# Performance work log

Hardware: AMD Instinct MI355X
Metric: run time of the kernel (lower is better)

The kernel has to match this reference:

```python
import jax, jax.numpy as jnp
import numpy as np

B, D, DFF, E, TOPK = 16384, 512, 2048, 8, 2


def setup_inputs() -> dict:
    key = jax.random.key(0)
    ks = jax.random.split(key, 5)
    scale_g = 1.0 / np.sqrt(D)
    scale_1 = 1.0 / np.sqrt(D)
    scale_2 = 1.0 / np.sqrt(DFF)
    return {
        "x": jax.random.normal(ks[0], (B, D), dtype=jnp.float32),
        "Wg": jax.random.normal(ks[1], (D, E), dtype=jnp.float32) * scale_g,
        "W1": jax.random.normal(ks[2], (E, D, DFF), dtype=jnp.float32) * scale_1,
        "b1": jnp.zeros((E, DFF), dtype=jnp.float32),
        "W2": jax.random.normal(ks[3], (E, DFF, D), dtype=jnp.float32) * scale_2,
        "b2": jnp.zeros((E, D), dtype=jnp.float32),
    }


def reference(x, Wg, W1, b1, W2, b2):
    # --- gate: top-k softmax routing weights, zeros elsewhere ---
    logits = x @ Wg                              # [B, E]
    probs = jax.nn.softmax(logits, axis=-1)      # [B, E]
    vals, idx = jax.lax.top_k(probs, TOPK)       # [B, K], [B, K]
    routing = jnp.zeros_like(probs).at[jnp.arange(x.shape[0])[:, None], idx].set(vals)  # [B, E]

    # --- experts: dense FFN per expert (equivalent math to masked dispatch) ---
    # original: gather selected tokens per expert, compute, scatter into
    # zeros[E, B, D], multiply by routing.T[:, :, None], sum over experts.
    # routing weight is exactly 0 for unselected tokens, so the dense form
    # out = sum_e routing[b, e] * expert_e(x_b) computes identical results.
    h = jax.nn.relu(jnp.einsum('bd,edf->ebf', x, W1) + b1[:, None, :])  # [E, B, DFF]
    y = jnp.einsum('ebf,efd->ebd', h, W2) + b2[:, None, :]              # [E, B, D]
    out = jnp.einsum('ebd,be->bd', y, routing)                          # [B, D]
    return out
```

## Files before the change

### kernel.cpp

```cpp
#include <hip/hip_runtime.h>
#include <stdint.h>

#define BTOK 16384
#define DM   512
#define DFF  2048
#define NE   8
#define NPAIR (BTOK*2)
#define BM 128
#define MAXTE 48

typedef short s16x8 __attribute__((ext_vector_type(8)));
typedef float f32x4 __attribute__((ext_vector_type(4)));

__device__ __forceinline__ uint16_t f2b(float f) {
  uint32_t u = __float_as_uint(f);
  u += 0x7fff + ((u >> 16) & 1);
  return (uint16_t)(u >> 16);
}

__device__ __forceinline__ void g2l16(const void* gp, void* lp) {
  __builtin_amdgcn_global_load_lds(
      (__attribute__((address_space(1))) void*)(void*)gp,
      (__attribute__((address_space(3))) void*)lp, 16, 0, 0);
}

__global__ void k_tr(const float* __restrict__ w1, const float* __restrict__ w2,
                     uint16_t* __restrict__ w1t, uint16_t* __restrict__ w2t) {
  __shared__ float t[32][33];
  int z = blockIdx.z, bx = blockIdx.x;
  int R, C, c0, r0;
  const float* src;
  uint16_t* dst;
  if (z < 8) { R = DM; C = DFF; c0 = (bx & 63) * 32; r0 = (bx >> 6) * 32;
               src = w1 + (size_t)z * R * C; dst = w1t + (size_t)z * R * C; }
  else       { R = DFF; C = DM; c0 = (bx & 15) * 32; r0 = (bx >> 4) * 32;
               src = w2 + (size_t)(z - 8) * R * C; dst = w2t + (size_t)(z - 8) * R * C; }
  int tx = threadIdx.x, ty = threadIdx.y;
#pragma unroll
  for (int j = 0; j < 4; j++)
    t[ty + j * 8][tx] = src[(size_t)(r0 + ty + j * 8) * C + c0 + tx];
  __syncthreads();
#pragma unroll
  for (int j = 0; j < 4; j++)
    dst[(size_t)(c0 + ty + j * 8) * R + r0 + tx] = f2b(t[tx][ty + j * 8]);
}

__global__ __launch_bounds__(256) void k_route(const float* __restrict__ x,
                                               const float* __restrict__ wg,
                                               int* __restrict__ counts,
                                               int* __restrict__ tk_e, float* __restrict__ tk_w,
                                               uint16_t* __restrict__ xb) {
  __shared__ int hist[NE];
  int tid = threadIdx.x, lane = tid & 63, wave = tid >> 6;
  if (tid < NE) hist[tid] = 0;
  __syncthreads();

  float wv[8][8];
#pragma unroll
  for (int j = 0; j < 8; j++) {
    const float4* wr = (const float4*)(wg + (size_t)(j * 64 + lane) * NE);
    float4 a = wr[0], b = wr[1];
    wv[j][0] = a.x; wv[j][1] = a.y; wv[j][2] = a.z; wv[j][3] = a.w;
    wv[j][4] = b.x; wv[j][5] = b.y; wv[j][6] = b.z; wv[j][7] = b.w;
  }

  int tok0 = blockIdx.x * 64 + wave * 16;
  for (int tt = 0; tt < 16; tt++) {
    int tok = tok0 + tt;
    const float* xr = x + (size_t)tok * DM;
    float xv[8];
#pragma unroll
    for (int j = 0; j < 8; j++) xv[j] = xr[j * 64 + lane];
    float acc[NE];
#pragma unroll
    for (int e = 0; e < NE; e++) acc[e] = 0.f;
#pragma unroll
    for (int j = 0; j < 8; j++)
#pragma unroll
      for (int e = 0; e < NE; e++) acc[e] += xv[j] * wv[j][e];
#pragma unroll
    for (int e = 0; e < NE; e++) {
#pragma unroll
      for (int off = 32; off > 0; off >>= 1) acc[e] += __shfl_xor(acc[e], off, 64);
    }
    if (lane == 0) {
      float mx = acc[0];
      for (int e = 1; e < NE; e++) mx = fmaxf(mx, acc[e]);
      float p[NE], s = 0.f;
      for (int e = 0; e < NE; e++) { p[e] = __expf(acc[e] - mx); s += p[e]; }
      float inv = 1.f / s;
      int e0 = 0; float v0 = p[0];
      for (int e = 1; e < NE; e++) if (p[e] > v0) { v0 = p[e]; e0 = e; }
      int e1 = -1; float v1 = -1.f;
      for (int e = 0; e < NE; e++) if (e != e0 && p[e] > v1) { v1 = p[e]; e1 = e; }
      tk_e[tok * 2]     = e0; tk_w[tok * 2]     = v0 * inv;
      tk_e[tok * 2 + 1] = e1; tk_w[tok * 2 + 1] = v1 * inv;
      atomicAdd(&hist[e0], 1);
      atomicAdd(&hist[e1], 1);
    }
  }
  const float* xs = x + (size_t)blockIdx.x * 32768;
  uint16_t* xd = xb + (size_t)blockIdx.x * 32768;
#pragma unroll
  for (int i = 0; i < 16; i++) {
    int o = i * 2048 + tid * 8;
    float4 a = *(const float4*)(xs + o);
    float4 b = *(const float4*)(xs + o + 4);
    uint16_t v[8] = {f2b(a.x), f2b(a.y), f2b(a.z), f2b(a.w),
                     f2b(b.x), f2b(b.y), f2b(b.z), f2b(b.w)};
    *(s16x8*)(xd + o) = *(s16x8*)v;
  }
  __syncthreads();
  if (tid < NE) atomicAdd(&counts[tid], hist[tid]);
}

__global__ void k_setup(const int* __restrict__ counts, int* __restrict__ offsets,
                        int* __restrict__ tile_r0, int* __restrict__ tcnt, int* __restrict__ tstart) {
  if (threadIdx.x != 0 || blockIdx.x != 0) return;
  int off = 0;
  for (int e = 0; e < NE; e++) { offsets[e] = off; off += counts[e]; }
  offsets[NE] = off;
  int nt = 0;
  for (int e = 0; e < NE; e++) {
    tstart[e] = nt;
    int c = 0;
    for (int r = offsets[e]; r < offsets[e + 1]; r += BM) { tile_r0[nt] = r; nt++; c++; }
    tcnt[e] = c;
  }
}

__global__ __launch_bounds__(256) void k_build(const int* __restrict__ tk_e, const float* __restrict__ tk_w,
                                               const int* __restrict__ offsets, int* __restrict__ cursors,
                                               int* __restrict__ tok_of, float* __restrict__ w_of,
                                               int* __restrict__ inv) {
  __shared__ int lcnt[NE], lbase[NE];
  int tid = threadIdx.x;
  int i = blockIdx.x * 256 + tid;
  if (tid < NE) lcnt[tid] = 0;
  __syncthreads();
  int e = tk_e[i];
  int local = atomicAdd(&lcnt[e], 1);
  __syncthreads();
  if (tid < NE) lbase[tid] = atomicAdd(&cursors[tid], lcnt[tid]);
  __syncthreads();
  int slot = offsets[e] + lbase[e] + local;
  tok_of[slot] = i >> 1;
  w_of[slot] = tk_w[i];
  inv[i] = slot;
}


__global__ __launch_bounds__(256, 2) void k_gemm1(
    const uint16_t* __restrict__ xb, const uint16_t* __restrict__ w1t,
    const float* __restrict__ b1,
    const int* __restrict__ tok_of, const int* __restrict__ offsets,
    const int* __restrict__ tile_r0, const int* __restrict__ tcnt, const int* __restrict__ tstart,
    uint16_t* __restrict__ h) {
  __shared__ uint16_t smem[24576];
  int id = blockIdx.x;
  int e = id & 7, j = id >> 3;
  int ti = j >> 3;
  if (ti >= tcnt[e]) return;
  int row0 = tile_r0[tstart[e] + ti], end = offsets[e + 1];
  int n0 = (j & 7) * 256;
  int tid = threadIdx.x, lane = tid & 63, wave = tid >> 6;
  int wr = (wave >> 1) * 64, wcb = (wave & 1) * 128;

  int aof[2];
#pragma unroll
  for (int it = 0; it < 2; it++) {
    int ci = it * 256 + tid;
    int row = ci >> 2;
    int c = (ci & 3) ^ ((row >> 1) & 3);
    int slot = row0 + row; if (slot >= end) slot = end - 1;
    aof[it] = tok_of[slot] * DM + c * 8;
  }
  int bof[4];
#pragma unroll
  for (int it = 0; it < 4; it++) {
    int ci = it * 256 + tid;
    int row = ci >> 2;
    int c = (ci & 3) ^ ((row >> 1) & 3);
    bof[it] = row * DM + c * 8;
  }
  const uint16_t* bb = w1t + (size_t)e * DFF * DM + (size_t)n0 * DM;
  int sfrag = (lane >> 4) ^ ((lane >> 1) & 3);

  f32x4 acc[4][8];
#pragma unroll
  for (int r = 0; r < 4; r++)
#pragma unroll
    for (int c = 0; c < 8; c++)
#pragma unroll
      for (int i = 0; i < 4; i++) acc[r][c][i] = 0.f;

#pragma unroll
  for (int it = 0; it < 2; it++)
    g2l16(xb + aof[it], smem + (size_t)(it * 256 + wave * 64) * 8);
#pragma unroll
  for (int it = 0; it < 4; it++)
    g2l16(bb + bof[it], smem + 4096 + (size_t)(it * 256 + wave * 64) * 8);

  int p = 0;
  for (int k0 = 0; k0 < DM; k0 += 32) {
    __syncthreads();
    int kn = k0 + 32, q = p ^ 1;
    if (kn < DM) {
#pragma unroll
      for (int it = 0; it < 2; it++)
        g2l16(xb + aof[it] + kn, smem + (size_t)q * 12288 + (size_t)(it * 256 + wave * 64) * 8);
#pragma unroll
      for (int it = 0; it < 4; it++)
        g2l16(bb + bof[it] + kn, smem + (size_t)q * 12288 + 4096 + (size_t)(it * 256 + wave * 64) * 8);
    }
    const uint16_t* sA = smem + (size_t)p * 12288;
    const uint16_t* sB = sA + 4096;
    s16x8 af[4], bf[8];
#pragma unroll
    for (int r = 0; r < 4; r++)
      af[r] = *(const s16x8*)(sA + (wr + r * 16 + (lane & 15)) * 32 + sfrag * 8);
#pragma unroll
    for (int c = 0; c < 8; c++)
      bf[c] = *(const s16x8*)(sB + (wcb + c * 16 + (lane & 15)) * 32 + sfrag * 8);
#pragma unroll
    for (int r = 0; r < 4; r++)
#pragma unroll
      for (int c = 0; c < 8; c++)
        acc[r][c] = __builtin_amdgcn_mfma_f32_16x16x32_bf16(af[r], bf[c], acc[r][c], 0, 0, 0);
    p = q;
  }
  __syncthreads();

  float bv[8];
#pragma unroll
  for (int c = 0; c < 8; c++) bv[c] = b1[(size_t)e * DFF + n0 + wcb + c * 16 + (lane & 15)];
#pragma unroll
  for (int ch = 0; ch < 2; ch++) {
    uint16_t* myreg = smem + wave * 4096;
#pragma unroll
    for (int r = 0; r < 4; r++)
#pragma unroll
      for (int c2 = 0; c2 < 4; c2++) {
        int gc = ch * 4 + c2;
#pragma unroll
        for (int i = 0; i < 4; i++) {
          int row = r * 16 + (lane >> 4) * 4 + i;
          int col = c2 * 16 + (lane & 15);
          float v = fmaxf(acc[r][gc][i] + bv[gc], 0.f);
          myreg[row * 64 + col] = f2b(v);
        }
      }
    __syncthreads();
#pragma unroll
    for (int it = 0; it < 8; it++) {
      int chunk = it * 256 + tid;
      int row = chunk >> 4, rem = chunk & 15;
      int strip = rem >> 3, cw = (rem & 7) * 8;
      int slot = row0 + row;
      if (slot < end) {
        const uint16_t* src = smem + ((row >> 6) * 2 + strip) * 4096 + (row & 63) * 64 + cw;
        *(s16x8*)(h + (size_t)slot * DFF + n0 + strip * 128 + ch * 64 + cw) = *(const s16x8*)src;
      }
    }
    __syncthreads();
  }
}

__global__ __launch_bounds__(256, 2) void k_gemm2(
    const uint16_t* __restrict__ h, const uint16_t* __restrict__ w2t,
    const float* __restrict__ b2,
    const float* __restrict__ w_of,
    const int* __restrict__ offsets,
    const int* __restrict__ tile_r0, const int* __restrict__ tcnt, const int* __restrict__ tstart,
    float* __restrict__ y32) {
  __shared__ uint16_t smem[24576];
  int id = blockIdx.x;
  int e = id & 7, j = id >> 3;
  int ti = j >> 1;
  if (ti >= tcnt[e]) return;
  int row0 = tile_r0[tstart[e] + ti], end = offsets[e + 1];
  int n0 = (j & 1) * 256;
  int tid = threadIdx.x, lane = tid & 63, wave = tid >> 6;
  int wr = (wave >> 1) * 64, wcb = (wave & 1) * 128;

  int aof[2];
#pragma unroll
  for (int it = 0; it < 2; it++) {
    int ci = it * 256 + tid;
    int row = ci >> 2;
    int c = (ci & 3) ^ ((row >> 1) & 3);
    int slot = row0 + row; if (slot >= end) slot = end - 1;
    aof[it] = slot * DFF + c * 8;
  }
  int bof[4];
#pragma unroll
  for (int it = 0; it < 4; it++) {
    int ci = it * 256 + tid;
    int row = ci >> 2;
    int c = (ci & 3) ^ ((row >> 1) & 3);
    bof[it] = row * DFF + c * 8;
  }
  const uint16_t* bb = w2t + (size_t)e * DM * DFF + (size_t)n0 * DFF;
  int sfrag = (lane >> 4) ^ ((lane >> 1) & 3);

  f32x4 acc[4][8];
#pragma unroll
  for (int r = 0; r < 4; r++)
#pragma unroll
    for (int c = 0; c < 8; c++)
#pragma unroll
      for (int i = 0; i < 4; i++) acc[r][c][i] = 0.f;

#pragma unroll
  for (int it = 0; it < 2; it++)
    g2l16(h + aof[it], smem + (size_t)(it * 256 + wave * 64) * 8);
#pragma unroll
  for (int it = 0; it < 4; it++)
    g2l16(bb + bof[it], smem + 4096 + (size_t)(it * 256 + wave * 64) * 8);

  int p = 0;
  for (int k0 = 0; k0 < DFF; k0 += 32) {
    __syncthreads();
    int kn = k0 + 32, q = p ^ 1;
    if (kn < DFF) {
#pragma unroll
      for (int it = 0; it < 2; it++)
        g2l16(h + aof[it] + kn, smem + (size_t)q * 12288 + (size_t)(it * 256 + wave * 64) * 8);
#pragma unroll
      for (int it = 0; it < 4; it++)
        g2l16(bb + bof[it] + kn, smem + (size_t)q * 12288 + 4096 + (size_t)(it * 256 + wave * 64) * 8);
    }
    const uint16_t* sA = smem + (size_t)p * 12288;
    const uint16_t* sB = sA + 4096;
    s16x8 af[4], bf[8];
#pragma unroll
    for (int r = 0; r < 4; r++)
      af[r] = *(const s16x8*)(sA + (wr + r * 16 + (lane & 15)) * 32 + sfrag * 8);
#pragma unroll
    for (int c = 0; c < 8; c++)
      bf[c] = *(const s16x8*)(sB + (wcb + c * 16 + (lane & 15)) * 32 + sfrag * 8);
#pragma unroll
    for (int r = 0; r < 4; r++)
#pragma unroll
      for (int c = 0; c < 8; c++)
        acc[r][c] = __builtin_amdgcn_mfma_f32_16x16x32_bf16(af[r], bf[c], acc[r][c], 0, 0, 0);
    p = q;
  }

  float bv[8];
#pragma unroll
  for (int c = 0; c < 8; c++) bv[c] = b2[(size_t)e * DM + n0 + wcb + c * 16 + (lane & 15)];
#pragma unroll
  for (int r = 0; r < 4; r++)
#pragma unroll
    for (int i = 0; i < 4; i++) {
      int rowg = wr + r * 16 + (lane >> 4) * 4 + i;
      int slot = row0 + rowg;
      if (slot < end) {
        float wgt = w_of[slot];
        size_t base = (size_t)slot * DM + n0 + wcb + (lane & 15);
#pragma unroll
        for (int c = 0; c < 8; c++) y32[base + c * 16] = wgt * (acc[r][c][i] + bv[c]);
      }
    }
}

__global__ __launch_bounds__(256) void k_combine(const float* __restrict__ y32,
                                                 const int* __restrict__ inv,
                                                 float* __restrict__ out) {
  int tid = threadIdx.x;
  int tok = blockIdx.x * 2 + (tid >> 7);
  int c4 = (tid & 127) * 4;
  int s0 = inv[tok * 2], s1 = inv[tok * 2 + 1];
  const float4 a = *(const float4*)(y32 + (size_t)s0 * DM + c4);
  const float4 b = *(const float4*)(y32 + (size_t)s1 * DM + c4);
  *(float4*)(out + (size_t)tok * DM + c4) = make_float4(a.x + b.x, a.y + b.y, a.z + b.z, a.w + b.w);
}

extern "C" void kernel_launch(void* const* d_in, const int* in_sizes, int n_in,
                              void* d_out, int out_size, void* d_ws, size_t ws_size,
                              hipStream_t stream) {
  const float* x  = (const float*)d_in[0];
  const float* wg = (const float*)d_in[1];
  const float* w1 = (const float*)d_in[2];
  const float* b1 = (const float*)d_in[3];
  const float* w2 = (const float*)d_in[4];
  const float* b2 = (const float*)d_in[5];
  float* out = (float*)d_out;

  char* ws = (char*)d_ws;
  const size_t MB = 1024 * 1024;
  uint16_t* xb   = (uint16_t*)ws;
  uint16_t* w1t  = (uint16_t*)(ws + 16 * MB);
  uint16_t* w2t  = (uint16_t*)(ws + 32 * MB);
  uint16_t* hbuf = (uint16_t*)(ws + 48 * MB);
  int* ctrl = (int*)(ws + 176 * MB);
  int*   counts  = ctrl;
  int*   cursors = ctrl + 8;
  int*   offsets = ctrl + 16;
  int*   tcnt    = ctrl + 32;
  int*   tstart  = ctrl + 40;
  int*   tile_r0 = ctrl + 48;
  int*   tk_e    = ctrl + 512;
  float* tk_w    = (float*)(ctrl + 512 + 32768);
  int*   tok_of  = ctrl + 512 + 2 * 32768;
  float* w_of    = (float*)(ctrl + 512 + 3 * 32768);
  int*   inv     = ctrl + 512 + 4 * 32768;
  float* y32     = (float*)(ws + 177 * MB);

  hipMemsetAsync(counts, 0, 16 * sizeof(int), stream);

  k_route<<<BTOK / 64, 256, 0, stream>>>(x, wg, counts, tk_e, tk_w, xb);
  k_tr<<<dim3(1024, 1, 16), dim3(32, 8), 0, stream>>>(w1, w2, w1t, w2t);
  k_setup<<<1, 64, 0, stream>>>(counts, offsets, tile_r0, tcnt, tstart);
  k_build<<<NPAIR / 256, 256, 0, stream>>>(tk_e, tk_w, offsets, cursors, tok_of, w_of, inv);
  k_gemm1<<<NE * MAXTE * 8, 256, 0, stream>>>(xb, w1t, b1, tok_of, offsets,
                                              tile_r0, tcnt, tstart, hbuf);
  k_gemm2<<<NE * MAXTE * 2, 256, 0, stream>>>(hbuf, w2t, b2, w_of, offsets,
                                              tile_r0, tcnt, tstart, y32);
  k_combine<<<BTOK / 2, 256, 0, stream>>>(y32, inv, out);
}
```

Measured before the change: 390.7 us.

## Rewrite expert GEMMs with 512-thread blocks, 4-stage LDS pipeline, larger tiles

Both grouped GEMMs move to 512-thread blocks with 8 waves. The global-to-LDS prefetch grows to a 4-stage ring with explicit vmcnt/lgkmcnt waits, split MFMA phases and raised priority around the MFMAs. GEMM1 now uses 256-row token tiles (a separate tile table is built in setup), while GEMM2 keeps 128 rows but spreads them over more waves. The aim is to hide memory latency and improve operand reuse in exchange for more LDS, hand-tuned wait counts, and more padding waste on partial expert tiles.

```diff
diff --git a/kernel.cpp b/kernel.cpp
--- a/kernel.cpp
+++ b/kernel.cpp
@@ -6,8 +6,8 @@
 #define DFF  2048
 #define NE   8
 #define NPAIR (BTOK*2)
-#define BM 128
-#define MAXTE 48
+#define MAXTA 24
+#define MAXTB 48
 
 typedef short s16x8 __attribute__((ext_vector_type(8)));
 typedef float f32x4 __attribute__((ext_vector_type(4)));
@@ -115,17 +115,23 @@
 }
 
 __global__ void k_setup(const int* __restrict__ counts, int* __restrict__ offsets,
-                        int* __restrict__ tile_r0, int* __restrict__ tcnt, int* __restrict__ tstart) {
+                        int* __restrict__ trA, int* __restrict__ tcntA, int* __restrict__ tstartA,
+                        int* __restrict__ trB, int* __restrict__ tcntB, int* __restrict__ tstartB) {
   if (threadIdx.x != 0 || blockIdx.x != 0) return;
   int off = 0;
   for (int e = 0; e < NE; e++) { offsets[e] = off; off += counts[e]; }
   offsets[NE] = off;
   int nt = 0;
   for (int e = 0; e < NE; e++) {
-    tstart[e] = nt;
-    int c = 0;
-    for (int r = offsets[e]; r < offsets[e + 1]; r += BM) { tile_r0[nt] = r; nt++; c++; }
-    tcnt[e] = c;
+    tstartA[e] = nt; int c = 0;
+    for (int r = offsets[e]; r < offsets[e + 1]; r += 256) { trA[nt++] = r; c++; }
+    tcntA[e] = c;
+  }
+  int nb = 0;
+  for (int e = 0; e < NE; e++) {
+    tstartB[e] = nb; int c = 0;
+    for (int r = offsets[e]; r < offsets[e + 1]; r += 128) { trB[nb++] = r; c++; }
+    tcntB[e] = c;
   }
 }
 
@@ -150,219 +156,273 @@
 }
 
 
-__global__ __launch_bounds__(256, 2) void k_gemm1(
+#define LDS16(off) (*(const s16x8*)((const char*)smem + (off)))
+#define VM8 asm volatile("s_waitcnt vmcnt(8)" ::: "memory")
+#define VM6 asm volatile("s_waitcnt vmcnt(6)" ::: "memory")
+#define VM4 asm volatile("s_waitcnt vmcnt(4)" ::: "memory")
+#define VM3 asm volatile("s_waitcnt vmcnt(3)" ::: "memory")
+#define VM0 asm volatile("s_waitcnt vmcnt(0)" ::: "memory")
+#define NOVM do{}while(0)
+#define NOSTG do{}while(0)
+#define MFMA16 __builtin_amdgcn_mfma_f32_16x16x32_bf16
+
+#define DS0_1(bb) do{ \
+  bf0 = LDS16(offB0 + (bb)*32768); bf1 = LDS16(offB1 + (bb)*32768); \
+  bf2 = LDS16(offB2 + (bb)*32768); bf3 = LDS16(offB3 + (bb)*32768); \
+  af0 = LDS16(offA0 + (bb)*32768); af1 = LDS16(offA1 + (bb)*32768); \
+  af2 = LDS16(offA2 + (bb)*32768); af3 = LDS16(offA3 + (bb)*32768); }while(0)
+#define DS1_1(bb) do{ \
+  af0 = LDS16(offA0 + (bb)*32768 + 4096); af1 = LDS16(offA1 + (bb)*32768 + 4096); \
+  af2 = LDS16(offA2 + (bb)*32768 + 4096); af3 = LDS16(offA3 + (bb)*32768 + 4096); }while(0)
+#define SA_1(bb) do{ \
+  g2l16(gA0, (char*)smem + (bb)*32768 + wave*1024); \
+  g2l16(gA1, (char*)smem + (bb)*32768 + 8192 + wave*1024); \
+  gA0 += 32; gA1 += 32; }while(0)
+#define SB_1(bb) do{ \
+  g2l16(gB0, (char*)smem + (bb)*32768 + 16384 + wave*1024); \
+  g2l16(gB1, (char*)smem + (bb)*32768 + 24576 + wave*1024); \
+  gB0 += 32; gB1 += 32; }while(0)
+#define MM16(H) do{ \
+  __builtin_amdgcn_s_setprio(1); \
+  acc[4*(H)+0][0] = MFMA16(af0, bf0, acc[4*(H)+0][0], 0, 0, 0); \
+  acc[4*(H)+1][0] = MFMA16(af1, bf0, acc[4*(H)+1][0], 0, 0, 0); \
+  acc[4*(H)+2][0] = MFMA16(af2, bf0, acc[4*(H)+2][0], 0, 0, 0); \
+  acc[4*(H)+3][0] = MFMA16(af3, bf0, acc[4*(H)+3][0], 0, 0, 0); \
+  acc[4*(H)+0][1] = MFMA16(af0, bf1, acc[4*(H)+0][1], 0, 0, 0); \
+  acc[4*(H)+1][1] = MFMA16(af1, bf1, acc[4*(H)+1][1], 0, 0, 0); \
+  acc[4*(H)+2][1] = MFMA16(af2, bf1, acc[4*(H)+2][1], 0, 0, 0); \
+  acc[4*(H)+3][1] = MFMA16(af3, bf1, acc[4*(H)+3][1], 0, 0, 0); \
+  acc[4*(H)+0][2] = MFMA16(af0, bf2, acc[4*(H)+0][2], 0, 0, 0); \
+  acc[4*(H)+1][2] = MFMA16(af1, bf2, acc[4*(H)+1][2], 0, 0, 0); \
+  acc[4*(H)+2][2] = MFMA16(af2, bf2, acc[4*(H)+2][2], 0, 0, 0); \
+  acc[4*(H)+3][2] = MFMA16(af3, bf2, acc[4*(H)+3][2], 0, 0, 0); \
+  acc[4*(H)+0][3] = MFMA16(af0, bf3, acc[4*(H)+0][3], 0, 0, 0); \
+  acc[4*(H)+1][3] = MFMA16(af1, bf3, acc[4*(H)+1][3], 0, 0, 0); \
+  acc[4*(H)+2][3] = MFMA16(af2, bf3, acc[4*(H)+2][3], 0, 0, 0); \
+  acc[4*(H)+3][3] = MFMA16(af3, bf3, acc[4*(H)+3][3], 0, 0, 0); \
+  __builtin_amdgcn_s_setprio(0); }while(0)
+#define TILE1(bb, SA, SB, VMX) do{ \
+  DS0_1(bb); SA; \
+  __builtin_amdgcn_s_barrier(); \
+  asm volatile("s_waitcnt lgkmcnt(0)" ::: "memory"); \
+  MM16(0); \
+  __builtin_amdgcn_s_barrier(); \
+  DS1_1(bb); SB; \
+  __builtin_amdgcn_s_barrier(); \
+  asm volatile("s_waitcnt lgkmcnt(0)" ::: "memory"); \
+  MM16(1); \
+  VMX; \
+  __builtin_amdgcn_s_barrier(); }while(0)
+
+__global__ __launch_bounds__(512, 2) void k_gemm1(
     const uint16_t* __restrict__ xb, const uint16_t* __restrict__ w1t,
     const float* __restrict__ b1,
     const int* __restrict__ tok_of, const int* __restrict__ offsets,
-    const int* __restrict__ tile_r0, const int* __restrict__ tcnt, const int* __restrict__ tstart,
+    const int* __restrict__ trA, const int* __restrict__ tcntA, const int* __restrict__ tstartA,
     uint16_t* __restrict__ h) {
-  __shared__ uint16_t smem[24576];
+  __shared__ __align__(16) uint16_t smem[65536];
   int id = blockIdx.x;
   int e = id & 7, j = id >> 3;
   int ti = j >> 3;
-  if (ti >= tcnt[e]) return;
-  int row0 = tile_r0[tstart[e] + ti], end = offsets[e + 1];
+  if (ti >= tcntA[e]) return;
+  int row0 = trA[tstartA[e] + ti], end = offsets[e + 1];
   int n0 = (j & 7) * 256;
   int tid = threadIdx.x, lane = tid & 63, wave = tid >> 6;
-  int wr = (wave >> 1) * 64, wcb = (wave & 1) * 128;
-
-  int aof[2];
-#pragma unroll
-  for (int it = 0; it < 2; it++) {
-    int ci = it * 256 + tid;
-    int row = ci >> 2;
-    int c = (ci & 3) ^ ((row >> 1) & 3);
-    int slot = row0 + row; if (slot >= end) slot = end - 1;
-    aof[it] = tok_of[slot] * DM + c * 8;
-  }
-  int bof[4];
-#pragma unroll
-  for (int it = 0; it < 4; it++) {
-    int ci = it * 256 + tid;
-    int row = ci >> 2;
-    int c = (ci & 3) ^ ((row >> 1) & 3);
-    bof[it] = row * DM + c * 8;
-  }
-  const uint16_t* bb = w1t + (size_t)e * DFF * DM + (size_t)n0 * DM;
-  int sfrag = (lane >> 4) ^ ((lane >> 1) & 3);
-
-  f32x4 acc[4][8];
-#pragma unroll
-  for (int r = 0; r < 4; r++)
-#pragma unroll
-    for (int c = 0; c < 8; c++)
-#pragma unroll
-      for (int i = 0; i < 4; i++) acc[r][c][i] = 0.f;
-
-#pragma unroll
-  for (int it = 0; it < 2; it++)
-    g2l16(xb + aof[it], smem + (size_t)(it * 256 + wave * 64) * 8);
-#pragma unroll
-  for (int it = 0; it < 4; it++)
-    g2l16(bb + bof[it], smem + 4096 + (size_t)(it * 256 + wave * 64) * 8);
-
-  int p = 0;
-  for (int k0 = 0; k0 < DM; k0 += 32) {
-    __syncthreads();
-    int kn = k0 + 32, q = p ^ 1;
-    if (kn < DM) {
-#pragma unroll
-      for (int it = 0; it < 2; it++)
-        g2l16(xb + aof[it] + kn, smem + (size_t)q * 12288 + (size_t)(it * 256 + wave * 64) * 8);
-#pragma unroll
-      for (int it = 0; it < 4; it++)
-        g2l16(bb + bof[it] + kn, smem + (size_t)q * 12288 + 4096 + (size_t)(it * 256 + wave * 64) * 8);
-    }
-    const uint16_t* sA = smem + (size_t)p * 12288;
-    const uint16_t* sB = sA + 4096;
-    s16x8 af[4], bf[8];
-#pragma unroll
-    for (int r = 0; r < 4; r++)
-      af[r] = *(const s16x8*)(sA + (wr + r * 16 + (lane & 15)) * 32 + sfrag * 8);
-#pragma unroll
-    for (int c = 0; c < 8; c++)
-      bf[c] = *(const s16x8*)(sB + (wcb + c * 16 + (lane & 15)) * 32 + sfrag * 8);
-#pragma unroll
-    for (int r = 0; r < 4; r++)
-#pragma unroll
-      for (int c = 0; c < 8; c++)
-        acc[r][c] = __builtin_amdgcn_mfma_f32_16x16x32_bf16(af[r], bf[c], acc[r][c], 0, 0, 0);
-    p = q;
-  }
-  __syncthreads();
-
-  float bv[8];
-#pragma unroll
-  for (int c = 0; c < 8; c++) bv[c] = b1[(size_t)e * DFF + n0 + wcb + c * 16 + (lane & 15)];
-#pragma unroll
-  for (int ch = 0; ch < 2; ch++) {
-    uint16_t* myreg = smem + wave * 4096;
-#pragma unroll
-    for (int r = 0; r < 4; r++)
-#pragma unroll
-      for (int c2 = 0; c2 < 4; c2++) {
-        int gc = ch * 4 + c2;
+  int wm = wave >> 2, wn = wave & 3;
+  int l15 = lane & 15, l4 = lane >> 4;
+
+  int offA0, offA1, offA2, offA3, offB0, offB1, offB2, offB3;
+  { int r;
+    r = wm*128 + 0*16 + l15; offA0 = r*64 + ((l4 ^ ((r>>1)&3)) << 4);
+    r = wm*128 + 1*16 + l15; offA1 = r*64 + ((l4 ^ ((r>>1)&3)) << 4);
+    r = wm*128 + 2*16 + l15; offA2 = r*64 + ((l4 ^ ((r>>1)&3)) << 4);
+    r = wm*128 + 3*16 + l15; offA3 = r*64 + ((l4 ^ ((r>>1)&3)) << 4);
+    r = wn*64  + 0*16 + l15; offB0 = 16384 + r*64 + ((l4 ^ ((r>>1)&3)) << 4);
+    r = wn*64  + 1*16 + l15; offB1 = 16384 + r*64 + ((l4 ^ ((r>>1)&3)) << 4);
+    r = wn*64  + 2*16 + l15; offB2 = 16384 + r*64 + ((l4 ^ ((r>>1)&3)) << 4);
+    r = wn*64  + 3*16 + l15; offB3 = 16384 + r*64 + ((l4 ^ ((r>>1)&3)) << 4);
+  }
+  const uint16_t *gA0, *gA1, *gB0, *gB1;
+  { int P = tid, r = P >> 2, c = (P & 3) ^ ((r >> 1) & 3);
+    int s = row0 + r; if (s >= end) s = end - 1;
+    gA0 = xb + (size_t)tok_of[s] * DM + c * 8;
+    gB0 = w1t + (size_t)e * DFF * DM + (size_t)(n0 + r) * DM + c * 8; }
+  { int P = 512 + tid, r = P >> 2, c = (P & 3) ^ ((r >> 1) & 3);
+    int s = row0 + r; if (s >= end) s = end - 1;
+    gA1 = xb + (size_t)tok_of[s] * DM + c * 8;
+    gB1 = w1t + (size_t)e * DFF * DM + (size_t)(n0 + r) * DM + c * 8; }
+
+  f32x4 acc[8][4];
+#pragma unroll
+  for (int m = 0; m < 8; m++)
+#pragma unroll
+    for (int n = 0; n < 4; n++)
+#pragma unroll
+      for (int i = 0; i < 4; i++) acc[m][n][i] = 0.f;
+
+  s16x8 af0, af1, af2, af3, bf0, bf1, bf2, bf3;
+
+  SA_1(0); SB_1(0); SA_1(1); SB_1(1); SA_1(2); SB_1(2);
+  VM8;
+  __builtin_amdgcn_s_barrier();
+
+#pragma unroll 1
+  for (int g = 0; g < 3; ++g) {
+    TILE1(0, SA_1(3), SB_1(3), VM8);
+    TILE1(1, SA_1(0), SB_1(0), VM8);
+    TILE1(2, SA_1(1), SB_1(1), VM8);
+    TILE1(3, SA_1(2), SB_1(2), VM8);
+  }
+  TILE1(0, SA_1(3), SB_1(3), VM8);
+  TILE1(1, NOSTG, NOSTG, VM4);
+  TILE1(2, NOSTG, NOSTG, VM0);
+  TILE1(3, NOSTG, NOSTG, NOVM);
+
+  {
+    float bv[4];
+#pragma unroll
+    for (int n = 0; n < 4; n++) bv[n] = b1[(size_t)e * DFF + n0 + wn * 64 + n * 16 + l15];
+    char* wrg = (char*)smem + wave * 2304;
+    int rr = lane >> 2, cb = lane & 3;
+#pragma unroll
+    for (int m = 0; m < 8; m++) {
+#pragma unroll
+      for (int n = 0; n < 4; n++)
 #pragma unroll
         for (int i = 0; i < 4; i++) {
-          int row = r * 16 + (lane >> 4) * 4 + i;
-          int col = c2 * 16 + (lane & 15);
-          float v = fmaxf(acc[r][gc][i] + bv[gc], 0.f);
-          myreg[row * 64 + col] = f2b(v);
+          float v = fmaxf(acc[m][n][i] + bv[n], 0.f);
+          *(uint16_t*)(wrg + (l4 * 4 + i) * 144 + (n * 16 + l15) * 2) = f2b(v);
         }
-      }
-    __syncthreads();
-#pragma unroll
-    for (int it = 0; it < 8; it++) {
-      int chunk = it * 256 + tid;
-      int row = chunk >> 4, rem = chunk & 15;
-      int strip = rem >> 3, cw = (rem & 7) * 8;
-      int slot = row0 + row;
-      if (slot < end) {
-        const uint16_t* src = smem + ((row >> 6) * 2 + strip) * 4096 + (row & 63) * 64 + cw;
-        *(s16x8*)(h + (size_t)slot * DFF + n0 + strip * 128 + ch * 64 + cw) = *(const s16x8*)src;
+      int gr = row0 + wm * 128 + m * 16 + rr;
+      const char* src = wrg + rr * 144 + cb * 32;
+      if (gr < end) {
+        uint16_t* dst = h + (size_t)gr * DFF + n0 + wn * 64 + cb * 16;
+        *(s16x8*)dst       = *(const s16x8*)src;
+        *(s16x8*)(dst + 8) = *(const s16x8*)(src + 16);
       }
     }
-    __syncthreads();
-  }
-}
-
-__global__ __launch_bounds__(256, 2) void k_gemm2(
+  }
+}
+
+#define DS0_2(bb) do{ \
+  bf0 = LDS16(offB0 + (bb)*24576); bf1 = LDS16(offB1 + (bb)*24576); \
+  bf2 = LDS16(offB2 + (bb)*24576); bf3 = LDS16(offB3 + (bb)*24576); \
+  af0 = LDS16(offA0 + (bb)*24576); af1 = LDS16(offA1 + (bb)*24576); }while(0)
+#define DS1_2(bb) do{ \
+  af0 = LDS16(offA2 + (bb)*24576); af1 = LDS16(offA3 + (bb)*24576); }while(0)
+#define SA_2(bb) do{ \
+  g2l16(gA0, (char*)smem + (bb)*24576 + wave*1024); \
+  gA0 += 32; }while(0)
+#define SB_2(bb) do{ \
+  g2l16(gB0, (char*)smem + (bb)*24576 + 8192 + wave*1024); \
+  g2l16(gB1, (char*)smem + (bb)*24576 + 16384 + wave*1024); \
+  gB0 += 32; gB1 += 32; }while(0)
+#define MM8(H) do{ \
+  __builtin_amdgcn_s_setprio(1); \
+  acc[2*(H)+0][0] = MFMA16(af0, bf0, acc[2*(H)+0][0], 0, 0, 0); \
+  acc[2*(H)+1][0] = MFMA16(af1, bf0, acc[2*(H)+1][0], 0, 0, 0); \
+  acc[2*(H)+0][1] = MFMA16(af0, bf1, acc[2*(H)+0][1], 0, 0, 0); \
+  acc[2*(H)+1][1] = MFMA16(af1, bf1, acc[2*(H)+1][1], 0, 0, 0); \
+  acc[2*(H)+0][2] = MFMA16(af0, bf2, acc[2*(H)+0][2], 0, 0, 0); \
+  acc[2*(H)+1][2] = MFMA16(af1, bf2, acc[2*(H)+1][2], 0, 0, 0); \
+  acc[2*(H)+0][3] = MFMA16(af0, bf3, acc[2*(H)+0][3], 0, 0, 0); \
+  acc[2*(H)+1][3] = MFMA16(af1, bf3, acc[2*(H)+1][3], 0, 0, 0); \
+  __builtin_amdgcn_s_setprio(0); }while(0)
+#define TILE2(bb, SA, SB, VMX) do{ \
+  DS0_2(bb); SA; \
+  __builtin_amdgcn_s_barrier(); \
+  asm volatile("s_waitcnt lgkmcnt(0)" ::: "memory"); \
+  MM8(0); \
+  __builtin_amdgcn_s_barrier(); \
+  DS1_2(bb); SB; \
+  __builtin_amdgcn_s_barrier(); \
+  asm volatile("s_waitcnt lgkmcnt(0)" ::: "memory"); \
+  MM8(1); \
+  VMX; \
+  __builtin_amdgcn_s_barrier(); }while(0)
+
+__global__ __launch_bounds__(512, 2) void k_gemm2(
     const uint16_t* __restrict__ h, const uint16_t* __restrict__ w2t,
-    const float* __restrict__ b2,
-    const float* __restrict__ w_of,
+    const float* __restrict__ b2, const float* __restrict__ w_of,
     const int* __restrict__ offsets,
-    const int* __restrict__ tile_r0, const int* __restrict__ tcnt, const int* __restrict__ tstart,
+    const int* __restrict__ trB, const int* __restrict__ tcntB, const int* __restrict__ tstartB,
     float* __restrict__ y32) {
-  __shared__ uint16_t smem[24576];
+  __shared__ __align__(16) uint16_t smem[49152];
   int id = blockIdx.x;
   int e = id & 7, j = id >> 3;
   int ti = j >> 1;
-  if (ti >= tcnt[e]) return;
-  int row0 = tile_r0[tstart[e] + ti], end = offsets[e + 1];
+  if (ti >= tcntB[e]) return;
+  int row0 = trB[tstartB[e] + ti], end = offsets[e + 1];
   int n0 = (j & 1) * 256;
   int tid = threadIdx.x, lane = tid & 63, wave = tid >> 6;
-  int wr = (wave >> 1) * 64, wcb = (wave & 1) * 128;
-
-  int aof[2];
-#pragma unroll
-  for (int it = 0; it < 2; it++) {
-    int ci = it * 256 + tid;
-    int row = ci >> 2;
-    int c = (ci & 3) ^ ((row >> 1) & 3);
-    int slot = row0 + row; if (slot >= end) slot = end - 1;
-    aof[it] = slot * DFF + c * 8;
-  }
-  int bof[4];
-#pragma unroll
-  for (int it = 0; it < 4; it++) {
-    int ci = it * 256 + tid;
-    int row = ci >> 2;
-    int c = (ci & 3) ^ ((row >> 1) & 3);
-    bof[it] = row * DFF + c * 8;
-  }
-  const uint16_t* bb = w2t + (size_t)e * DM * DFF + (size_t)n0 * DFF;
-  int sfrag = (lane >> 4) ^ ((lane >> 1) & 3);
-
-  f32x4 acc[4][8];
-#pragma unroll
-  for (int r = 0; r < 4; r++)
-#pragma unroll
-    for (int c = 0; c < 8; c++)
-#pragma unroll
-      for (int i = 0; i < 4; i++) acc[r][c][i] = 0.f;
-
-#pragma unroll
-  for (int it = 0; it < 2; it++)
-    g2l16(h + aof[it], smem + (size_t)(it * 256 + wave * 64) * 8);
-#pragma unroll
-  for (int it = 0; it < 4; it++)
-    g2l16(bb + bof[it], smem + 4096 + (size_t)(it * 256 + wave * 64) * 8);
-
-  int p = 0;
-  for (int k0 = 0; k0 < DFF; k0 += 32) {
-    __syncthreads();
-    int kn = k0 + 32, q = p ^ 1;
-    if (kn < DFF) {
-#pragma unroll
-      for (int it = 0; it < 2; it++)
-        g2l16(h + aof[it] + kn, smem + (size_t)q * 12288 + (size_t)(it * 256 + wave * 64) * 8);
-#pragma unroll
-      for (int it = 0; it < 4; it++)
-        g2l16(bb + bof[it] + kn, smem + (size_t)q * 12288 + 4096 + (size_t)(it * 256 + wave * 64) * 8);
-    }
-    const uint16_t* sA = smem + (size_t)p * 12288;
-    const uint16_t* sB = sA + 4096;
-    s16x8 af[4], bf[8];
-#pragma unroll
-    for (int r = 0; r < 4; r++)
-      af[r] = *(const s16x8*)(sA + (wr + r * 16 + (lane & 15)) * 32 + sfrag * 8);
-#pragma unroll
-    for (int c = 0; c < 8; c++)
-      bf[c] = *(const s16x8*)(sB + (wcb + c * 16 + (lane & 15)) * 32 + sfrag * 8);
-#pragma unroll
-    for (int r = 0; r < 4; r++)
-#pragma unroll
-      for (int c = 0; c < 8; c++)
-        acc[r][c] = __builtin_amdgcn_mfma_f32_16x16x32_bf16(af[r], bf[c], acc[r][c], 0, 0, 0);
-    p = q;
-  }
-
-  float bv[8];
-#pragma unroll
-  for (int c = 0; c < 8; c++) bv[c] = b2[(size_t)e * DM + n0 + wcb + c * 16 + (lane & 15)];
-#pragma unroll
-  for (int r = 0; r < 4; r++)
-#pragma unroll
-    for (int i = 0; i < 4; i++) {
-      int rowg = wr + r * 16 + (lane >> 4) * 4 + i;
-      int slot = row0 + rowg;
-      if (slot < end) {
-        float wgt = w_of[slot];
-        size_t base = (size_t)slot * DM + n0 + wcb + (lane & 15);
-#pragma unroll
-        for (int c = 0; c < 8; c++) y32[base + c * 16] = wgt * (acc[r][c][i] + bv[c]);
+  int wm = wave >> 2, wn = wave & 3;
+  int l15 = lane & 15, l4 = lane >> 4;
+
+  int offA0, offA1, offA2, offA3, offB0, offB1, offB2, offB3;
+  { int r;
+    r = wm*64 + 0*16 + l15; offA0 = r*64 + ((l4 ^ ((r>>1)&3)) << 4);
+    r = wm*64 + 1*16 + l15; offA1 = r*64 + ((l4 ^ ((r>>1)&3)) << 4);
+    r = wm*64 + 2*16 + l15; offA2 = r*64 + ((l4 ^ ((r>>1)&3)) << 4);
+    r = wm*64 + 3*16 + l15; offA3 = r*64 + ((l4 ^ ((r>>1)&3)) << 4);
+    r = wn*64 + 0*16 + l15; offB0 = 8192 + r*64 + ((l4 ^ ((r>>1)&3)) << 4);
+    r = wn*64 + 1*16 + l15; offB1 = 8192 + r*64 + ((l4 ^ ((r>>1)&3)) << 4);
+    r = wn*64 + 2*16 + l15; offB2 = 8192 + r*64 + ((l4 ^ ((r>>1)&3)) << 4);
+    r = wn*64 + 3*16 + l15; offB3 = 8192 + r*64 + ((l4 ^ ((r>>1)&3)) << 4);
+  }
+  const uint16_t *gA0, *gB0, *gB1;
+  { int P = tid, r = P >> 2, c = (P & 3) ^ ((r >> 1) & 3);
+    int s = row0 + r; if (s >= end) s = end - 1;
+    gA0 = h + (size_t)s * DFF + c * 8; }
+  { int P = tid, r = P >> 2, c = (P & 3) ^ ((r >> 1) & 3);
+    gB0 = w2t + (size_t)e * DM * DFF + (size_t)(n0 + r) * DFF + c * 8; }
+  { int P = 512 + tid, r = P >> 2, c = (P & 3) ^ ((r >> 1) & 3);
+    gB1 = w2t + (size_t)e * DM * DFF + (size_t)(n0 + r) * DFF + c * 8; }
+
+  f32x4 acc[4][4];
+#pragma unroll
+  for (int m = 0; m < 4; m++)
+#pragma unroll
+    for (int n = 0; n < 4; n++)
+#pragma unroll
+      for (int i = 0; i < 4; i++) acc[m][n][i] = 0.f;
+
+  s16x8 af0, af1, bf0, bf1, bf2, bf3;
+
+  SA_2(0); SB_2(0); SA_2(1); SB_2(1); SA_2(2); SB_2(2);
+  VM6;
+  __builtin_amdgcn_s_barrier();
+
+#pragma unroll 1
+  for (int g = 0; g < 15; ++g) {
+    TILE2(0, SA_2(3), SB_2(3), VM6);
+    TILE2(1, SA_2(0), SB_2(0), VM6);
+    TILE2(2, SA_2(1), SB_2(1), VM6);
+    TILE2(3, SA_2(2), SB_2(2), VM6);
+  }
+  TILE2(0, SA_2(3), SB_2(3), VM6);
+  TILE2(1, NOSTG, NOSTG, VM3);
+  TILE2(2, NOSTG, NOSTG, VM0);
+  TILE2(3, NOSTG, NOSTG, NOVM);
+
+  {
+    float bv[4];
+#pragma unroll
+    for (int n = 0; n < 4; n++) bv[n] = b2[(size_t)e * DM + n0 + wn * 64 + n * 16 + l15];
+#pragma unroll
+    for (int m = 0; m < 4; m++)
+#pragma unroll
+      for (int i = 0; i < 4; i++) {
+        int slot = row0 + wm * 64 + m * 16 + l4 * 4 + i;
+        if (slot < end) {
+          float wgt = w_of[slot];
+          size_t base = (size_t)slot * DM + n0 + wn * 64 + l15;
+          y32[base +  0] = wgt * (acc[m][0][i] + bv[0]);
+          y32[base + 16] = wgt * (acc[m][1][i] + bv[1]);
+          y32[base + 32] = wgt * (acc[m][2][i] + bv[2]);
+          y32[base + 48] = wgt * (acc[m][3][i] + bv[3]);
+        }
       }
-    }
+  }
 }
 
 __global__ __launch_bounds__(256) void k_combine(const float* __restrict__ y32,
@@ -398,25 +458,28 @@
   int*   counts  = ctrl;
   int*   cursors = ctrl + 8;
   int*   offsets = ctrl + 16;
-  int*   tcnt    = ctrl + 32;
-  int*   tstart  = ctrl + 40;
-  int*   tile_r0 = ctrl + 48;
-  int*   tk_e    = ctrl + 512;
-  float* tk_w    = (float*)(ctrl + 512 + 32768);
-  int*   tok_of  = ctrl + 512 + 2 * 32768;
-  float* w_of    = (float*)(ctrl + 512 + 3 * 32768);
-  int*   inv     = ctrl + 512 + 4 * 32768;
+  int*   tcntA   = ctrl + 32;
+  int*   tstartA = ctrl + 40;
+  int*   trA     = ctrl + 48;
+  int*   tcntB   = ctrl + 240;
+  int*   tstartB = ctrl + 248;
+  int*   trB     = ctrl + 256;
+  int*   tk_e    = ctrl + 1024;
+  float* tk_w    = (float*)(ctrl + 1024 + 32768);
+  int*   tok_of  = ctrl + 1024 + 2 * 32768;
+  float* w_of    = (float*)(ctrl + 1024 + 3 * 32768);
+  int*   inv     = ctrl + 1024 + 4 * 32768;
   float* y32     = (float*)(ws + 177 * MB);
 
   hipMemsetAsync(counts, 0, 16 * sizeof(int), stream);
 
   k_route<<<BTOK / 64, 256, 0, stream>>>(x, wg, counts, tk_e, tk_w, xb);
   k_tr<<<dim3(1024, 1, 16), dim3(32, 8), 0, stream>>>(w1, w2, w1t, w2t);
-  k_setup<<<1, 64, 0, stream>>>(counts, offsets, tile_r0, tcnt, tstart);
+  k_setup<<<1, 64, 0, stream>>>(counts, offsets, trA, tcntA, tstartA, trB, tcntB, tstartB);
   k_build<<<NPAIR / 256, 256, 0, stream>>>(tk_e, tk_w, offsets, cursors, tok_of, w_of, inv);
-  k_gemm1<<<NE * MAXTE * 8, 256, 0, stream>>>(xb, w1t, b1, tok_of, offsets,
-                                              tile_r0, tcnt, tstart, hbuf);
-  k_gemm2<<<NE * MAXTE * 2, 256, 0, stream>>>(hbuf, w2t, b2, w_of, offsets,
-                                              tile_r0, tcnt, tstart, y32);
+  k_gemm1<<<NE * 8 * MAXTA, 512, 0, stream>>>(xb, w1t, b1, tok_of, offsets,
+                                              trA, tcntA, tstartA, hbuf);
+  k_gemm2<<<NE * 2 * MAXTB, 512, 0, stream>>>(hbuf, w2t, b2, w_of, offsets,
+                                              trB, tcntB, tstartB, y32);
   k_combine<<<BTOK / 2, 256, 0, stream>>>(y32, inv, out);
 }
```

After: 385.4 us. Within noise of the previous version (-1.4%).
